# Optimization experiments

Hardware: AMD Instinct MI355X
Metric: run time of the kernel (lower is better)

## Reference

```python
import jax, jax.numpy as jnp
import numpy as np

N, E = 100000, 800000
D_IN, D_H, D_EMB = 64, 64, 64
L, S = 2, 4
NOISE_SCALE, MIN_U = 0.1, 1e-6


def _xavier(k, shape):
    lim = float(np.sqrt(6.0 / (shape[0] + shape[1])))
    return jax.random.uniform(k, shape, jnp.float32, -lim, lim)


def setup_inputs():
    key = jax.random.key(0)
    ks = jax.random.split(key, 7)
    x = jax.random.normal(ks[0], (N, D_IN), jnp.float32)
    edge_index = jax.random.randint(ks[1], (2, E), 0, N)
    parent_mask = jax.random.bernoulli(ks[2], 0.7, (E,))
    Wi = _xavier(ks[3], (D_IN, D_H))
    bi = jnp.zeros((D_H,), jnp.float32)
    msg_W = jnp.stack([_xavier(jax.random.fold_in(ks[4], l), (2 * D_H, D_H)) for l in range(L)])
    msg_b = jnp.zeros((L, D_H), jnp.float32)
    upd_W = jnp.stack([_xavier(jax.random.fold_in(ks[5], l), (2 * D_H, D_H)) for l in range(L)])
    upd_b = jnp.zeros((L, D_H), jnp.float32)
    Wf = _xavier(ks[6], (D_H, D_EMB))
    bf = jnp.zeros((D_EMB,), jnp.float32)
    return dict(x=x, edge_index=edge_index, parent_mask=parent_mask, Wi=Wi, bi=bi,
                msg_W=msg_W, msg_b=msg_b, upd_W=upd_W, upd_b=upd_b, Wf=Wf, bf=bf)


def _gnn(x, src, dst, mask_f, cnt_inv, Wi, bi, msg_W, msg_b, upd_W, upd_b, Wf, bf):
    # input_proj -> relu, then L rounds of (gather -> message linear -> masked
    # scatter-mean -> update linear -> relu), then final_proj.
    h = jax.nn.relu(x @ Wi + bi)
    for l in range(L):
        Wm, Wu = msg_W[l], upd_W[l]
        # message = Linear(concat(x_i, x_j)); x_i = h[dst] (target), x_j = h[src] (source)
        msg = h[dst] @ Wm[:D_H] + h[src] @ Wm[D_H:] + msg_b[l]  # [E, D_H]
        agg = jax.ops.segment_sum(msg * mask_f[:, None], dst, num_segments=N) * cnt_inv[:, None]
        # update = Linear(concat(x, aggr_out))
        h = jax.nn.relu(h @ Wu[:D_H] + agg @ Wu[D_H:] + upd_b[l])
    return h @ Wf + bf  # [N, D_EMB]


def reference(x, edge_index, parent_mask, Wi, bi, msg_W, msg_b, upd_W, upd_b, Wf, bf):
    src, dst = edge_index[0], edge_index[1]
    mask_f = parent_mask.astype(x.dtype)
    # scatter-mean over causal-parent edges only (0 for nodes without parents, as in PyG)
    cnt = jax.ops.segment_sum(mask_f, dst, num_segments=N)
    cnt_inv = 1.0 / jnp.maximum(cnt, 1.0)
    params = (Wi, bi, msg_W, msg_b, upd_W, upd_b, Wf, bf)
    causal_z = _gnn(x, src, dst, mask_f, cnt_inv, *params)
    # Monte Carlo uncertainty: S perturbed causal embeddings, trace of sample covariance
    noise = jax.random.normal(jax.random.key(42), (S, N, D_IN), x.dtype) * NOISE_SCALE
    zs = jax.lax.map(lambda n: _gnn(x + n, src, dst, mask_f, cnt_inv, *params), noise)  # [S, N, D_EMB]
    mean = zs.mean(axis=0)
    u = jnp.sum((zs - mean[None]) ** 2, axis=(0, 2)) / (S - 1)
    u = jnp.maximum(u, MIN_U)
    return causal_z, u
```

## Files before the change

kernel.cpp:

```cpp
#include <hip/hip_runtime.h>
#include <stdint.h>

#define NN 100000
#define EE 800000
#define GEMM_BX 1563
#define WSTR 72
#define SLAB ((size_t)NN * 64)

typedef unsigned short u16;
typedef __attribute__((ext_vector_type(8))) short bf16x8;
typedef __attribute__((ext_vector_type(4))) float f32x4;

__device__ __forceinline__ uint32_t f2bf(float f) {
  uint32_t u = __float_as_uint(f);
  return (u + 0x7fffu + ((u >> 16) & 1u)) >> 16;
}

__device__ __forceinline__ void tf_round(uint32_t& x0, uint32_t& x1, int r) {
  x0 += x1;
  x1 = (x1 << r) | (x1 >> (32 - r));
  x1 ^= x0;
}

__device__ __forceinline__ void threefry_0_42(uint32_t c0, uint32_t c1,
                                              uint32_t& o0, uint32_t& o1) {
  const uint32_t ks0 = 0u, ks1 = 42u, ks2 = 0x1BD11BDAu ^ 42u;
  uint32_t x0 = c0 + ks0, x1 = c1 + ks1;
  tf_round(x0, x1, 13); tf_round(x0, x1, 15); tf_round(x0, x1, 26); tf_round(x0, x1, 6);
  x0 += ks1; x1 += ks2 + 1u;
  tf_round(x0, x1, 17); tf_round(x0, x1, 29); tf_round(x0, x1, 16); tf_round(x0, x1, 24);
  x0 += ks2; x1 += ks0 + 2u;
  tf_round(x0, x1, 13); tf_round(x0, x1, 15); tf_round(x0, x1, 26); tf_round(x0, x1, 6);
  x0 += ks0; x1 += ks1 + 3u;
  tf_round(x0, x1, 17); tf_round(x0, x1, 29); tf_round(x0, x1, 16); tf_round(x0, x1, 24);
  x0 += ks1; x1 += ks2 + 4u;
  tf_round(x0, x1, 13); tf_round(x0, x1, 15); tf_round(x0, x1, 26); tf_round(x0, x1, 6);
  x0 += ks2; x1 += ks0 + 5u;
  o0 = x0; o1 = x1;
}

__device__ __forceinline__ float noise_val(int s, int n, int d) {
  uint32_t f = (uint32_t)s * 6400000u + (uint32_t)n * 64u + (uint32_t)d;
  uint32_t o0, o1;
  threefry_0_42(0u, f, o0, o1);
  uint32_t bits = o0 ^ o1;
  float v = __uint_as_float((bits >> 9) | 0x3f800000u) - 1.0f;
  const float LO = -0.99999994f;
  float u = v * 2.0f + LO;
  u = fmaxf(u, LO);
  float w = -__logf(fmaf(-u, u, 1.0f));
  float ww = w - 2.5f;
  float p = 2.81022636e-08f;
  p = fmaf(p, ww, 3.43273939e-07f);
  p = fmaf(p, ww, -3.5233877e-06f);
  p = fmaf(p, ww, -4.39150654e-06f);
  p = fmaf(p, ww, 0.00021858087f);
  p = fmaf(p, ww, -0.00125372503f);
  p = fmaf(p, ww, -0.00417768164f);
  p = fmaf(p, ww, 0.246640727f);
  p = fmaf(p, ww, 1.50140941f);
  if (__any(w >= 5.0f)) {
    float ws = sqrtf(w) - 3.0f;
    float p2 = -0.000200214257f;
    p2 = fmaf(p2, ws, 0.000100950558f);
    p2 = fmaf(p2, ws, 0.00134934322f);
    p2 = fmaf(p2, ws, -0.00367342844f);
    p2 = fmaf(p2, ws, 0.00573950773f);
    p2 = fmaf(p2, ws, -0.0076224613f);
    p2 = fmaf(p2, ws, 0.00943887047f);
    p2 = fmaf(p2, ws, 1.00167406f);
    p2 = fmaf(p2, ws, 2.83297682f);
    p = (w < 5.0f) ? p : p2;
  }
  return 0.141421356f * (p * u);
}

__device__ __forceinline__ int mask_at(const void* m, int e, int mode) {
  if (mode == 0) return ((const int*)m)[e] != 0;
  if (mode == 1) return ((const unsigned char*)m)[e] != 0;
  return ((const float*)m)[e] != 0.0f;
}

__global__ void k_detect(const unsigned* mw, int* mode_out) {
  __shared__ int nonbin, nonfloat;
  if (threadIdx.x == 0) { nonbin = 0; nonfloat = 0; }
  __syncthreads();
  int lb = 0, lf = 0;
  for (int i = threadIdx.x; i < 4096; i += 256) {
    unsigned v = mw[i];
    if (v > 1u) lb = 1;
    if (v != 0u && v != 0x3F800000u) lf = 1;
  }
  if (lb) atomicOr(&nonbin, 1);
  if (lf) atomicOr(&nonfloat, 1);
  __syncthreads();
  if (threadIdx.x == 0)
    mode_out[0] = (nonbin == 0) ? 0 : ((nonfloat == 0) ? 2 : 1);
}

__global__ void k_count(const void* mask, const int* dst, int* cnt, const int* mode_p) {
  int e = blockIdx.x * 256 + threadIdx.x;
  if (e >= EE) return;
  if (mask_at(mask, e, *mode_p)) atomicAdd(&cnt[dst[e]], 1);
}

__global__ void k_scan_a(const int* cnt, int* blockSums) {
  __shared__ int sd[256];
  int t = threadIdx.x;
  int base = blockIdx.x * 1024 + t * 4;
  int s = 0;
  #pragma unroll
  for (int j = 0; j < 4; ++j) {
    int i = base + j;
    if (i < NN) s += cnt[i];
  }
  sd[t] = s;
  __syncthreads();
  for (int off = 128; off > 0; off >>= 1) {
    if (t < off) sd[t] += sd[t + off];
    __syncthreads();
  }
  if (t == 0) blockSums[blockIdx.x] = sd[0];
}

__global__ void k_scan_b(int* blockSums, int nb, int* total_out) {
  __shared__ int sd[128];
  int t = threadIdx.x;
  int v = (t < nb) ? blockSums[t] : 0;
  sd[t] = v;
  __syncthreads();
  for (int off = 1; off < 128; off <<= 1) {
    int x = (t >= off) ? sd[t - off] : 0;
    __syncthreads();
    sd[t] += x;
    __syncthreads();
  }
  if (t < nb) blockSums[t] = sd[t] - v;
  if (t == 0) total_out[0] = sd[127];
}

__global__ void k_scan_c(const int* cnt, const int* blockOffs, int* row_ptr,
                         int* cursor, float* cinv) {
  __shared__ int sd[256];
  int t = threadIdx.x;
  int base = blockIdx.x * 1024 + t * 4;
  int v[4], s = 0;
  #pragma unroll
  for (int j = 0; j < 4; ++j) {
    int i = base + j;
    v[j] = (i < NN) ? cnt[i] : 0;
    s += v[j];
  }
  sd[t] = s;
  __syncthreads();
  for (int off = 1; off < 256; off <<= 1) {
    int x = (t >= off) ? sd[t - off] : 0;
    __syncthreads();
    sd[t] += x;
    __syncthreads();
  }
  int excl = sd[t] - s + blockOffs[blockIdx.x];
  #pragma unroll
  for (int j = 0; j < 4; ++j) {
    int i = base + j;
    if (i < NN) {
      row_ptr[i] = excl;
      cursor[i] = excl;
      cinv[i] = 1.0f / fmaxf((float)v[j], 1.0f);
    }
    excl += v[j];
  }
}

__global__ void k_fill(const void* mask, const int* src, const int* dst,
                       int* cursor, int* col, const int* mode_p) {
  int e = blockIdx.x * 256 + threadIdx.x;
  if (e >= EE) return;
  if (mask_at(mask, e, *mode_p)) {
    int p = atomicAdd(&cursor[dst[e]], 1);
    col[p] = src[e];
  }
}

__global__ void k_prep(const float* msg_W, const float* msg_b, const float* upd_W,
                       const float* Wi, const float* Wf,
                       u16* Wu1T, u16* A1T, u16* A2T, float* C1,
                       u16* WiT, u16* WfT) {
  int t = threadIdx.x;
  if (blockIdx.x == 2) {
    for (int o = t; o < 4096; o += 256) {
      int k = o >> 6, n = o & 63;
      WiT[n * 64 + k] = (u16)f2bf(Wi[k * 64 + n]);
      WfT[n * 64 + k] = (u16)f2bf(Wf[k * 64 + n]);
    }
    return;
  }
  int l = blockIdx.x;
  const float* WmT = msg_W + l * 8192;
  const float* WmB = WmT + 4096;
  const float* Wu1 = upd_W + l * 8192;
  const float* Wu2 = Wu1 + 4096;
  for (int o = t; o < 4096; o += 256) {
    int a = o >> 6, b = o & 63;
    float a1 = 0.f, a2 = 0.f;
    for (int j = 0; j < 64; ++j) {
      float w2 = Wu2[j * 64 + b];
      a1 = fmaf(WmT[a * 64 + j], w2, a1);
      a2 = fmaf(WmB[a * 64 + j], w2, a2);
    }
    A1T[l * 4096 + b * 64 + a]  = (u16)f2bf(a1);
    A2T[l * 4096 + b * 64 + a]  = (u16)f2bf(a2);
    Wu1T[l * 4096 + b * 64 + a] = (u16)f2bf(Wu1[a * 64 + b]);
  }
  if (t < 64) {
    float acc = 0.f;
    for (int j = 0; j < 64; ++j) acc = fmaf(msg_b[l * 64 + j], Wu2[j * 64 + t], acc);
    C1[l * 64 + t] = acc;
  }
}

__device__ __forceinline__ void mm4(const u16* lW, int m16, int q,
                                    bf16x8 a0, bf16x8 a1, f32x4 (&acc)[4]) {
  #pragma unroll
  for (int nt = 0; nt < 4; ++nt) {
    const u16* wp = lW + (nt * 16 + m16) * WSTR + q * 8;
    bf16x8 b0 = *(const bf16x8*)(wp);
    bf16x8 b1 = *(const bf16x8*)(wp + 32);
    acc[nt] = __builtin_amdgcn_mfma_f32_16x16x32_bf16(a0, b0, acc[nt], 0, 0, 0);
    acc[nt] = __builtin_amdgcn_mfma_f32_16x16x32_bf16(a1, b1, acc[nt], 0, 0, 0);
  }
}

__device__ __forceinline__ void stage_W(const u16* __restrict__ WT, u16* lW) {
  int t = threadIdx.x;
  int r = t >> 2, seg = (t & 3) * 16;
  const uint4* p = (const uint4*)(WT + r * 64 + seg);
  uint4 a = p[0], b = p[1];
  *(uint4*)(lW + r * WSTR + seg) = a;
  *(uint4*)(lW + r * WSTR + seg + 8) = b;
}

__device__ __forceinline__ void stage_H(const u16* __restrict__ Hin, int R0, u16* lT) {
  int t = threadIdx.x;
  int r = t >> 2, seg = (t & 3) * 16;
  int gr = R0 + r;
  uint4 a = {0, 0, 0, 0}, b = {0, 0, 0, 0};
  if (gr < NN) {
    const uint4* p = (const uint4*)(Hin + (size_t)gr * 64 + seg);
    a = p[0]; b = p[1];
  }
  *(uint4*)(lT + r * WSTR + seg) = a;
  *(uint4*)(lT + r * WSTR + seg + 8) = b;
}

__global__ __launch_bounds__(256) void k_input(const float* __restrict__ x,
                                               const u16* __restrict__ WiT,
                                               const float* __restrict__ bi,
                                               u16* __restrict__ HoutB) {
  __shared__ __align__(16) u16 lT[64 * WSTR];
  __shared__ __align__(16) u16 lW[64 * WSTR];
  __shared__ float lB[64];
  int t = threadIdx.x;
  int R0 = blockIdx.x * 64;
  int inst = blockIdx.y;
  u16* Hout = HoutB + (size_t)inst * SLAB;
  {
    int r = t >> 2, seg = (t & 3) * 16;
    int gr = R0 + r;
    float v[16];
    if (gr < NN) {
      const float4* xp = (const float4*)(x + (size_t)gr * 64 + seg);
      #pragma unroll
      for (int qq = 0; qq < 4; ++qq) {
        float4 f = xp[qq];
        v[qq * 4 + 0] = f.x; v[qq * 4 + 1] = f.y;
        v[qq * 4 + 2] = f.z; v[qq * 4 + 3] = f.w;
      }
      if (inst > 0) {
        int s = inst - 1;
        #pragma unroll
        for (int j = 0; j < 16; ++j) v[j] += noise_val(s, gr, seg + j);
      }
    } else {
      #pragma unroll
      for (int j = 0; j < 16; ++j) v[j] = 0.f;
    }
    uint32_t pk[8];
    #pragma unroll
    for (int j = 0; j < 8; ++j)
      pk[j] = f2bf(v[2 * j]) | (f2bf(v[2 * j + 1]) << 16);
    uint4 A = {pk[0], pk[1], pk[2], pk[3]};
    uint4 B = {pk[4], pk[5], pk[6], pk[7]};
    *(uint4*)(lT + r * WSTR + seg) = A;
    *(uint4*)(lT + r * WSTR + seg + 8) = B;
  }
  stage_W(WiT, lW);
  if (t < 64) lB[t] = bi[t];
  __syncthreads();
  int l = t & 63, w = t >> 6;
  int m16 = l & 15, q = l >> 4;
  const u16* aRow = lT + (w * 16 + m16) * WSTR + q * 8;
  bf16x8 fa0 = *(const bf16x8*)(aRow);
  bf16x8 fa1 = *(const bf16x8*)(aRow + 32);
  f32x4 acc[4] = {{0.f, 0.f, 0.f, 0.f}, {0.f, 0.f, 0.f, 0.f},
                  {0.f, 0.f, 0.f, 0.f}, {0.f, 0.f, 0.f, 0.f}};
  mm4(lW, m16, q, fa0, fa1, acc);
  #pragma unroll
  for (int nt = 0; nt < 4; ++nt) {
    int c = nt * 16 + m16;
    #pragma unroll
    for (int r_ = 0; r_ < 4; ++r_) {
      int row = w * 16 + q * 4 + r_;
      int gr = R0 + row;
      if (gr < NN) {
        float vv = fmaxf(acc[nt][r_] + lB[c], 0.f);
        Hout[(size_t)gr * 64 + c] = (u16)f2bf(vv);
      }
    }
  }
}

__global__ __launch_bounds__(256) void k_layer(const u16* __restrict__ HinB,
                                               u16* __restrict__ HoutB,
                                               const int* __restrict__ row_ptr,
                                               const int* __restrict__ col,
                                               const int* __restrict__ cnt,
                                               const float* __restrict__ cinv,
                                               const u16* __restrict__ Wu1T,
                                               const u16* __restrict__ A1T,
                                               const u16* __restrict__ A2T,
                                               const float* __restrict__ b0,
                                               const float* __restrict__ c1) {
  __shared__ __align__(16) u16 lS0[64 * WSTR];
  __shared__ __align__(16) u16 lS1[64 * WSTR];
  __shared__ __align__(16) u16 lW[64 * WSTR];
  __shared__ float lB[128];
  __shared__ float lG[64];
  int t = threadIdx.x;
  int R0 = blockIdx.x * 64;
  int instBase = blockIdx.y * 2;
  bool two = (instBase + 1) < 5;
  const u16* Hin0 = HinB + (size_t)instBase * SLAB;
  const u16* Hin1 = Hin0 + (two ? SLAB : 0);
  u16* Hout0 = HoutB + (size_t)instBase * SLAB;
  u16* Hout1 = Hout0 + SLAB;

  stage_W(Wu1T, lW);
  if (t < 64) {
    lB[t] = b0[t];
    lB[64 + t] = c1[t];
    int gr = R0 + t;
    lG[t] = (gr < NN && cnt[gr] > 0) ? 1.f : 0.f;
  }

  int l = t & 63, w = t >> 6;
  int m16 = l & 15, q = l >> 4;
  int arow = w * 16 + m16;
  int gra = R0 + arow;
  bf16x8 zz = {0, 0, 0, 0, 0, 0, 0, 0};
  bf16x8 fa0_0 = zz, fa1_0 = zz, fa0_1 = zz, fa1_1 = zz;
  if (gra < NN) {
    const u16* ap = Hin0 + (size_t)gra * 64 + q * 8;
    fa0_0 = *(const bf16x8*)(ap);
    fa1_0 = *(const bf16x8*)(ap + 32);
    if (two) {
      const u16* ap1 = Hin1 + (size_t)gra * 64 + q * 8;
      fa0_1 = *(const bf16x8*)(ap1);
      fa1_1 = *(const bf16x8*)(ap1 + 32);
    }
  }

  {
    int wv = t >> 6, sub = (t >> 4) & 3, f0 = (t & 15) << 2;
    const u16* hb0 = Hin0 + f0;
    const u16* hb1 = Hin1 + f0;
    #pragma unroll
    for (int bb = 0; bb < 4; ++bb) {
      int r = wv * 16 + bb * 4 + sub;
      int n = R0 + r;
      float g0 = 0.f, g1 = 0.f, g2 = 0.f, g3 = 0.f;
      float h0 = 0.f, h1 = 0.f, h2 = 0.f, h3 = 0.f;
      if (n < NN) {
        int e = row_ptr[n], end = row_ptr[n + 1];
        for (; e < end; e += 8) {
          int last = end - 1;
          size_t offv[8];
          #pragma unroll
          for (int j = 0; j < 8; ++j) {
            int ee = e + j;
            ee = (ee < last) ? ee : last;
            offv[j] = (size_t)col[ee] * 64;
          }
          uint2 P[8];
          #pragma unroll
          for (int j = 0; j < 8; ++j) P[j] = *(const uint2*)(hb0 + offv[j]);
          uint2 Q[8];
          if (two) {
            #pragma unroll
            for (int j = 0; j < 8; ++j) Q[j] = *(const uint2*)(hb1 + offv[j]);
          }
          #pragma unroll
          for (int j = 1; j < 8; ++j) {
            bool ok = (e + j) < end;
            P[j].x = ok ? P[j].x : 0u;
            P[j].y = ok ? P[j].y : 0u;
            if (two) {
              Q[j].x = ok ? Q[j].x : 0u;
              Q[j].y = ok ? Q[j].y : 0u;
            }
          }
          #pragma unroll
          for (int j = 0; j < 8; ++j) {
            g0 += __uint_as_float(P[j].x << 16);
            g1 += __uint_as_float(P[j].x & 0xffff0000u);
            g2 += __uint_as_float(P[j].y << 16);
            g3 += __uint_as_float(P[j].y & 0xffff0000u);
          }
          if (two) {
            #pragma unroll
            for (int j = 0; j < 8; ++j) {
              h0 += __uint_as_float(Q[j].x << 16);
              h1 += __uint_as_float(Q[j].x & 0xffff0000u);
              h2 += __uint_as_float(Q[j].y << 16);
              h3 += __uint_as_float(Q[j].y & 0xffff0000u);
            }
          }
        }
        float ci = cinv[n];
        g0 *= ci; g1 *= ci; g2 *= ci; g3 *= ci;
        h0 *= ci; h1 *= ci; h2 *= ci; h3 *= ci;
      }
      uint2 pk;
      pk.x = f2bf(g0) | (f2bf(g1) << 16);
      pk.y = f2bf(g2) | (f2bf(g3) << 16);
      *(uint2*)(lS0 + r * WSTR + f0) = pk;
      if (two) {
        uint2 pk2;
        pk2.x = f2bf(h0) | (f2bf(h1) << 16);
        pk2.y = f2bf(h2) | (f2bf(h3) << 16);
        *(uint2*)(lS1 + r * WSTR + f0) = pk2;
      }
    }
  }
  __syncthreads();

  float gA = lG[arow];
  f32x4 acc0[4] = {{0.f, 0.f, 0.f, 0.f}, {0.f, 0.f, 0.f, 0.f},
                   {0.f, 0.f, 0.f, 0.f}, {0.f, 0.f, 0.f, 0.f}};
  f32x4 acc1[4] = {{0.f, 0.f, 0.f, 0.f}, {0.f, 0.f, 0.f, 0.f},
                   {0.f, 0.f, 0.f, 0.f}, {0.f, 0.f, 0.f, 0.f}};
  mm4(lW, m16, q, fa0_0, fa1_0, acc0);
  if (two) mm4(lW, m16, q, fa0_1, fa1_1, acc1);
  __syncthreads();
  stage_W(A1T, lW);
  __syncthreads();
  {
    bf16x8 ga0 = (gA != 0.f) ? fa0_0 : zz;
    bf16x8 ga1 = (gA != 0.f) ? fa1_0 : zz;
    mm4(lW, m16, q, ga0, ga1, acc0);
    if (two) {
      bf16x8 gb0 = (gA != 0.f) ? fa0_1 : zz;
      bf16x8 gb1 = (gA != 0.f) ? fa1_1 : zz;
      mm4(lW, m16, q, gb0, gb1, acc1);
    }
  }
  __syncthreads();
  stage_W(A2T, lW);
  __syncthreads();
  {
    const u16* sRow = lS0 + arow * WSTR + q * 8;
    bf16x8 fs0 = *(const bf16x8*)(sRow);
    bf16x8 fs1 = *(const bf16x8*)(sRow + 32);
    mm4(lW, m16, q, fs0, fs1, acc0);
    if (two) {
      const u16* sRow1 = lS1 + arow * WSTR + q * 8;
      bf16x8 ft0 = *(const bf16x8*)(sRow1);
      bf16x8 ft1 = *(const bf16x8*)(sRow1 + 32);
      mm4(lW, m16, q, ft0, ft1, acc1);
    }
  }
  #pragma unroll
  for (int nt = 0; nt < 4; ++nt) {
    int c = nt * 16 + m16;
    #pragma unroll
    for (int r_ = 0; r_ < 4; ++r_) {
      int row = w * 16 + q * 4 + r_;
      int gr = R0 + row;
      if (gr < NN) {
        float bias = lB[c] + lG[row] * lB[64 + c];
        float v0 = fmaxf(acc0[nt][r_] + bias, 0.f);
        Hout0[(size_t)gr * 64 + c] = (u16)f2bf(v0);
        if (two) {
          float v1 = fmaxf(acc1[nt][r_] + bias, 0.f);
          Hout1[(size_t)gr * 64 + c] = (u16)f2bf(v1);
        }
      }
    }
  }
}

__global__ __launch_bounds__(256) void k_final(const u16* __restrict__ HinB,
                                               const u16* __restrict__ WfT,
                                               const float* __restrict__ bfv,
                                               float* __restrict__ outCausal,
                                               float* __restrict__ out_u) {
  __shared__ __align__(16) u16 lT[64 * WSTR];
  __shared__ __align__(16) u16 lW[64 * WSTR];
  __shared__ float lB[64];
  int t = threadIdx.x;
  int R0 = blockIdx.x * 64;
  stage_W(WfT, lW);
  if (t < 64) lB[t] = bfv[t];
  int l = t & 63, w = t >> 6;
  int m16 = l & 15, q = l >> 4;
  float s1[16], s2[16];
  #pragma unroll
  for (int j = 0; j < 16; ++j) { s1[j] = 0.f; s2[j] = 0.f; }

  for (int inst = 0; inst < 5; ++inst) {
    __syncthreads();
    stage_H(HinB + (size_t)inst * SLAB, R0, lT);
    __syncthreads();
    const u16* aRow = lT + (w * 16 + m16) * WSTR + q * 8;
    bf16x8 fa0 = *(const bf16x8*)(aRow);
    bf16x8 fa1 = *(const bf16x8*)(aRow + 32);
    f32x4 acc[4] = {{0.f, 0.f, 0.f, 0.f}, {0.f, 0.f, 0.f, 0.f},
                    {0.f, 0.f, 0.f, 0.f}, {0.f, 0.f, 0.f, 0.f}};
    mm4(lW, m16, q, fa0, fa1, acc);
    #pragma unroll
    for (int nt = 0; nt < 4; ++nt) {
      int c = nt * 16 + m16;
      #pragma unroll
      for (int r_ = 0; r_ < 4; ++r_) {
        float z = acc[nt][r_] + lB[c];
        if (inst == 0) {
          int gr = R0 + w * 16 + q * 4 + r_;
          if (gr < NN) outCausal[(size_t)gr * 64 + c] = z;
        } else {
          s1[nt * 4 + r_] += z;
          s2[nt * 4 + r_] = fmaf(z, z, s2[nt * 4 + r_]);
        }
      }
    }
  }
  #pragma unroll
  for (int r_ = 0; r_ < 4; ++r_) {
    float pr = 0.f;
    #pragma unroll
    for (int nt = 0; nt < 4; ++nt) {
      float a = s1[nt * 4 + r_];
      pr += s2[nt * 4 + r_] - 0.25f * a * a;
    }
    #pragma unroll
    for (int msk = 1; msk < 16; msk <<= 1)
      pr += __shfl_xor(pr, msk, 64);
    if (m16 == 0) {
      int gr = R0 + w * 16 + q * 4 + r_;
      if (gr < NN) out_u[gr] = fmaxf(pr * (1.0f / 3.0f), 1e-6f);
    }
  }
}

extern "C" void kernel_launch(void* const* d_in, const int* in_sizes, int n_in,
                              void* d_out, int out_size, void* d_ws, size_t ws_size,
                              hipStream_t stream) {
  const float* x      = (const float*)d_in[0];
  const int*   eidx   = (const int*)d_in[1];
  const void*  mask   = d_in[2];
  const float* Wi     = (const float*)d_in[3];
  const float* bi     = (const float*)d_in[4];
  const float* msg_W  = (const float*)d_in[5];
  const float* msg_b  = (const float*)d_in[6];
  const float* upd_W  = (const float*)d_in[7];
  const float* upd_b  = (const float*)d_in[8];
  const float* Wf     = (const float*)d_in[9];
  const float* bfv    = (const float*)d_in[10];

  const int* src = eidx;
  const int* dst = eidx + EE;

  char* ws = (char*)d_ws;
  size_t off = 0;
  auto alloc = [&](size_t bytes) -> void* {
    void* p = ws + off;
    off += (bytes + 255) & ~(size_t)255;
    return p;
  };

  int*   cnt     = (int*)alloc(NN * sizeof(int));
  float* cinv    = (float*)alloc(NN * sizeof(float));
  int*   row_ptr = (int*)alloc((NN + 1) * sizeof(int));
  int*   cursor  = (int*)alloc(NN * sizeof(int));
  int*   col     = (int*)alloc(EE * sizeof(int));
  int*   bsums   = (int*)alloc(128 * sizeof(int));
  int*   mode_p  = (int*)alloc(sizeof(int));
  u16*   Wu1T    = (u16*)alloc(2 * 4096 * sizeof(u16));
  u16*   A1T     = (u16*)alloc(2 * 4096 * sizeof(u16));
  u16*   A2T     = (u16*)alloc(2 * 4096 * sizeof(u16));
  u16*   WiT     = (u16*)alloc(4096 * sizeof(u16));
  u16*   WfT     = (u16*)alloc(4096 * sizeof(u16));
  float* C1      = (float*)alloc(2 * 64 * sizeof(float));
  u16*   HA      = (u16*)alloc(5 * SLAB * sizeof(u16));
  u16*   HB      = (u16*)alloc(5 * SLAB * sizeof(u16));

  float* out_causal = (float*)d_out;
  float* out_u      = (float*)d_out + SLAB;

  k_detect<<<1, 256, 0, stream>>>((const unsigned*)mask, mode_p);
  hipMemsetAsync(cnt, 0, NN * sizeof(int), stream);
  k_count<<<EE / 256, 256, 0, stream>>>(mask, dst, cnt, mode_p);
  const int SCAN_BLKS = (NN + 1023) / 1024;
  k_scan_a<<<SCAN_BLKS, 256, 0, stream>>>(cnt, bsums);
  k_scan_b<<<1, 128, 0, stream>>>(bsums, SCAN_BLKS, row_ptr + NN);
  k_scan_c<<<SCAN_BLKS, 256, 0, stream>>>(cnt, bsums, row_ptr, cursor, cinv);
  k_fill<<<EE / 256, 256, 0, stream>>>(mask, src, dst, cursor, col, mode_p);

  k_prep<<<3, 256, 0, stream>>>(msg_W, msg_b, upd_W, Wi, Wf,
                                Wu1T, A1T, A2T, C1, WiT, WfT);

  dim3 g5(GEMM_BX, 5);
  dim3 gl(GEMM_BX, 3);
  k_input<<<g5, 256, 0, stream>>>(x, WiT, bi, HA);
  k_layer<<<gl, 256, 0, stream>>>(HA, HB, row_ptr, col, cnt, cinv,
                                  Wu1T, A1T, A2T, upd_b, C1);
  k_layer<<<gl, 256, 0, stream>>>(HB, HA, row_ptr, col, cnt, cinv,
                                  Wu1T + 4096, A1T + 4096, A2T + 4096,
                                  upd_b + 64, C1 + 64);
  k_final<<<GEMM_BX, 256, 0, stream>>>(HA, WfT, bfv, out_causal, out_u);

  (void)in_sizes; (void)n_in; (void)out_size; (void)ws_size;
}
```

Baseline: 507.9 us.

## Stage block edge lists in LDS and widen gather to 16-byte loads

The layer kernel now loads the block's row_ptr slice and, when the block's edges fit within 2304 entries, copies its col indices into LDS, reusing the weight buffer before the weights are staged. The neighbour gather is restructured so 8 threads cover one row with uint4 (8 bf16) loads instead of 16 threads with uint2, with 4 edges unrolled per iteration. lG is derived from row_ptr, so the cnt array is no longer read. The intent is fewer, wider global transactions and cheaper index fetches, at the cost of an extra barrier and weight staging that now happens after aggregation.

```diff
diff --git a/kernel.cpp b/kernel.cpp
--- a/kernel.cpp
+++ b/kernel.cpp
@@ -6,6 +6,7 @@
 #define GEMM_BX 1563
 #define WSTR 72
 #define SLAB ((size_t)NN * 64)
+#define EDGE_CAP 2304
 
 typedef unsigned short u16;
 typedef __attribute__((ext_vector_type(8))) short bf16x8;
@@ -324,7 +325,6 @@
                                                u16* __restrict__ HoutB,
                                                const int* __restrict__ row_ptr,
                                                const int* __restrict__ col,
-                                               const int* __restrict__ cnt,
                                                const float* __restrict__ cinv,
                                                const u16* __restrict__ Wu1T,
                                                const u16* __restrict__ A1T,
@@ -336,6 +336,9 @@
   __shared__ __align__(16) u16 lW[64 * WSTR];
   __shared__ float lB[128];
   __shared__ float lG[64];
+  __shared__ int   lRP[65];
+  int* lEdge = (int*)lW;
+
   int t = threadIdx.x;
   int R0 = blockIdx.x * 64;
   int instBase = blockIdx.y * 2;
@@ -345,13 +348,121 @@
   u16* Hout0 = HoutB + (size_t)instBase * SLAB;
   u16* Hout1 = Hout0 + SLAB;
 
-  stage_W(Wu1T, lW);
+  if (t < 65) {
+    int idx = R0 + t;
+    if (idx > NN) idx = NN;
+    lRP[t] = row_ptr[idx];
+  }
   if (t < 64) {
     lB[t] = b0[t];
     lB[64 + t] = c1[t];
-    int gr = R0 + t;
-    lG[t] = (gr < NN && cnt[gr] > 0) ? 1.f : 0.f;
-  }
+  }
+  __syncthreads();
+
+  int e0 = lRP[0];
+  int nE = lRP[64] - e0;
+  bool inLds = (nE <= EDGE_CAP);
+  if (inLds) {
+    for (int i = t; i < nE; i += 256) lEdge[i] = col[e0 + i];
+  }
+  if (t < 64) lG[t] = (lRP[t + 1] > lRP[t]) ? 1.f : 0.f;
+  __syncthreads();
+
+  {
+    int sub = t >> 3, lane8 = t & 7;
+    int f0 = lane8 * 8;
+    const u16* hb0 = Hin0 + f0;
+    const u16* hb1 = Hin1 + f0;
+    #pragma unroll
+    for (int bb = 0; bb < 2; ++bb) {
+      int r = bb * 32 + sub;
+      int n = R0 + r;
+      float g[8], h[8];
+      #pragma unroll
+      for (int j = 0; j < 8; ++j) { g[j] = 0.f; h[j] = 0.f; }
+      if (n < NN) {
+        int e = lRP[r], end = lRP[r + 1];
+        int last = end - 1;
+        for (; e < end; e += 4) {
+          int idx4[4];
+          #pragma unroll
+          for (int j = 0; j < 4; ++j) {
+            int ee = e + j;
+            ee = (ee < last) ? ee : last;
+            idx4[j] = inLds ? lEdge[ee - e0] : col[ee];
+          }
+          uint4 P[4];
+          #pragma unroll
+          for (int j = 0; j < 4; ++j)
+            P[j] = *(const uint4*)(hb0 + ((unsigned)idx4[j] << 6));
+          uint4 Q[4];
+          if (two) {
+            #pragma unroll
+            for (int j = 0; j < 4; ++j)
+              Q[j] = *(const uint4*)(hb1 + ((unsigned)idx4[j] << 6));
+          }
+          #pragma unroll
+          for (int j = 1; j < 4; ++j) {
+            bool ok = (e + j) < end;
+            P[j].x = ok ? P[j].x : 0u;
+            P[j].y = ok ? P[j].y : 0u;
+            P[j].z = ok ? P[j].z : 0u;
+            P[j].w = ok ? P[j].w : 0u;
+            if (two) {
+              Q[j].x = ok ? Q[j].x : 0u;
+              Q[j].y = ok ? Q[j].y : 0u;
+              Q[j].z = ok ? Q[j].z : 0u;
+              Q[j].w = ok ? Q[j].w : 0u;
+            }
+          }
+          #pragma unroll
+          for (int j = 0; j < 4; ++j) {
+            uint4 v = P[j];
+            g[0] += __uint_as_float(v.x << 16);
+            g[1] += __uint_as_float(v.x & 0xffff0000u);
+            g[2] += __uint_as_float(v.y << 16);
+            g[3] += __uint_as_float(v.y & 0xffff0000u);
+            g[4] += __uint_as_float(v.z << 16);
+            g[5] += __uint_as_float(v.z & 0xffff0000u);
+            g[6] += __uint_as_float(v.w << 16);
+            g[7] += __uint_as_float(v.w & 0xffff0000u);
+          }
+          if (two) {
+            #pragma unroll
+            for (int j = 0; j < 4; ++j) {
+              uint4 v = Q[j];
+              h[0] += __uint_as_float(v.x << 16);
+              h[1] += __uint_as_float(v.x & 0xffff0000u);
+              h[2] += __uint_as_float(v.y << 16);
+              h[3] += __uint_as_float(v.y & 0xffff0000u);
+              h[4] += __uint_as_float(v.z << 16);
+              h[5] += __uint_as_float(v.z & 0xffff0000u);
+              h[6] += __uint_as_float(v.w << 16);
+              h[7] += __uint_as_float(v.w & 0xffff0000u);
+            }
+          }
+        }
+        float ci = cinv[n];
+        #pragma unroll
+        for (int j = 0; j < 8; ++j) { g[j] *= ci; h[j] *= ci; }
+      }
+      uint4 pk;
+      pk.x = f2bf(g[0]) | (f2bf(g[1]) << 16);
+      pk.y = f2bf(g[2]) | (f2bf(g[3]) << 16);
+      pk.z = f2bf(g[4]) | (f2bf(g[5]) << 16);
+      pk.w = f2bf(g[6]) | (f2bf(g[7]) << 16);
+      *(uint4*)(lS0 + r * WSTR + f0) = pk;
+      if (two) {
+        uint4 pk2;
+        pk2.x = f2bf(h[0]) | (f2bf(h[1]) << 16);
+        pk2.y = f2bf(h[2]) | (f2bf(h[3]) << 16);
+        pk2.z = f2bf(h[4]) | (f2bf(h[5]) << 16);
+        pk2.w = f2bf(h[6]) | (f2bf(h[7]) << 16);
+        *(uint4*)(lS1 + r * WSTR + f0) = pk2;
+      }
+    }
+  }
+  __syncthreads();
 
   int l = t & 63, w = t >> 6;
   int m16 = l & 15, q = l >> 4;
@@ -370,78 +481,7 @@
     }
   }
 
-  {
-    int wv = t >> 6, sub = (t >> 4) & 3, f0 = (t & 15) << 2;
-    const u16* hb0 = Hin0 + f0;
-    const u16* hb1 = Hin1 + f0;
-    #pragma unroll
-    for (int bb = 0; bb < 4; ++bb) {
-      int r = wv * 16 + bb * 4 + sub;
-      int n = R0 + r;
-      float g0 = 0.f, g1 = 0.f, g2 = 0.f, g3 = 0.f;
-      float h0 = 0.f, h1 = 0.f, h2 = 0.f, h3 = 0.f;
-      if (n < NN) {
-        int e = row_ptr[n], end = row_ptr[n + 1];
-        for (; e < end; e += 8) {
-          int last = end - 1;
-          size_t offv[8];
-          #pragma unroll
-          for (int j = 0; j < 8; ++j) {
-            int ee = e + j;
-            ee = (ee < last) ? ee : last;
-            offv[j] = (size_t)col[ee] * 64;
-          }
-          uint2 P[8];
-          #pragma unroll
-          for (int j = 0; j < 8; ++j) P[j] = *(const uint2*)(hb0 + offv[j]);
-          uint2 Q[8];
-          if (two) {
-            #pragma unroll
-            for (int j = 0; j < 8; ++j) Q[j] = *(const uint2*)(hb1 + offv[j]);
-          }
-          #pragma unroll
-          for (int j = 1; j < 8; ++j) {
-            bool ok = (e + j) < end;
-            P[j].x = ok ? P[j].x : 0u;
-            P[j].y = ok ? P[j].y : 0u;
-            if (two) {
-              Q[j].x = ok ? Q[j].x : 0u;
-              Q[j].y = ok ? Q[j].y : 0u;
-            }
-          }
-          #pragma unroll
-          for (int j = 0; j < 8; ++j) {
-            g0 += __uint_as_float(P[j].x << 16);
-            g1 += __uint_as_float(P[j].x & 0xffff0000u);
-            g2 += __uint_as_float(P[j].y << 16);
-            g3 += __uint_as_float(P[j].y & 0xffff0000u);
-          }
-          if (two) {
-            #pragma unroll
-            for (int j = 0; j < 8; ++j) {
-              h0 += __uint_as_float(Q[j].x << 16);
-              h1 += __uint_as_float(Q[j].x & 0xffff0000u);
-              h2 += __uint_as_float(Q[j].y << 16);
-              h3 += __uint_as_float(Q[j].y & 0xffff0000u);
-            }
-          }
-        }
-        float ci = cinv[n];
-        g0 *= ci; g1 *= ci; g2 *= ci; g3 *= ci;
-        h0 *= ci; h1 *= ci; h2 *= ci; h3 *= ci;
-      }
-      uint2 pk;
-      pk.x = f2bf(g0) | (f2bf(g1) << 16);
-      pk.y = f2bf(g2) | (f2bf(g3) << 16);
-      *(uint2*)(lS0 + r * WSTR + f0) = pk;
-      if (two) {
-        uint2 pk2;
-        pk2.x = f2bf(h0) | (f2bf(h1) << 16);
-        pk2.y = f2bf(h2) | (f2bf(h3) << 16);
-        *(uint2*)(lS1 + r * WSTR + f0) = pk2;
-      }
-    }
-  }
+  stage_W(Wu1T, lW);
   __syncthreads();
 
   float gA = lG[arow];
@@ -621,9 +661,9 @@
   dim3 g5(GEMM_BX, 5);
   dim3 gl(GEMM_BX, 3);
   k_input<<<g5, 256, 0, stream>>>(x, WiT, bi, HA);
-  k_layer<<<gl, 256, 0, stream>>>(HA, HB, row_ptr, col, cnt, cinv,
+  k_layer<<<gl, 256, 0, stream>>>(HA, HB, row_ptr, col, cinv,
                                   Wu1T, A1T, A2T, upd_b, C1);
-  k_layer<<<gl, 256, 0, stream>>>(HB, HA, row_ptr, col, cnt, cinv,
+  k_layer<<<gl, 256, 0, stream>>>(HB, HA, row_ptr, col, cinv,
                                   Wu1T + 4096, A1T + 4096, A2T + 4096,
                                   upd_b + 64, C1 + 64);
   k_final<<<GEMM_BX, 256, 0, stream>>>(HA, WfT, bfv, out_causal, out_u);
```

After: 473.0 us. 6.9% less time.
